# Kernel tuning notes

Measured on AMD Instinct MI355X. Metric: run time of the kernel, lower is better.

Reference implementation:

```python
import jax, jax.numpy as jnp
import numpy as np

N_NODES = 20000
N_EDGES = 120000
N_GRAPHS = 512
F_IN = 300
NHID = 256
NHID_FF = 256
NOUT = 768
SLOPE = 0.2
EPS = 1e-16


def _p(key, shape, scale=0.05):
    return jax.random.normal(key, shape, dtype=jnp.float32) * scale


def setup_inputs() -> dict:
    key = jax.random.key(0)
    ks = jax.random.split(key, 24)
    inp = {
        "x": jax.random.normal(ks[0], (N_NODES, F_IN), dtype=jnp.float32),
        "edge_index": jax.random.randint(ks[1], (2, N_EDGES), 0, N_NODES, dtype=jnp.int64) if False else jax.random.randint(ks[1], (2, N_EDGES), 0, N_NODES).astype(jnp.int32),
        "batch": jnp.sort(jax.random.randint(ks[2], (N_NODES,), 0, N_GRAPHS)).astype(jnp.int32),
        # conv1: in=300 -> heads=4, C=256, concat
        "c1_wl": _p(ks[3], (4 * NHID, F_IN)),
        "c1_wr": _p(ks[4], (4 * NHID, F_IN)),
        "c1_att": _p(ks[5], (4, NHID)),
        "c1_b": jnp.zeros((4 * NHID,), jnp.float32),
        # conv2: in=1024 -> heads=4, C=256, concat
        "c2_wl": _p(ks[6], (4 * NHID, 4 * NHID)),
        "c2_wr": _p(ks[7], (4 * NHID, 4 * NHID)),
        "c2_att": _p(ks[8], (4, NHID)),
        "c2_b": jnp.zeros((4 * NHID,), jnp.float32),
        # conv3: in=1024 -> heads=6, C=256, mean (concat=False)
        "c3_wl": _p(ks[9], (6 * NHID_FF, 4 * NHID)),
        "c3_wr": _p(ks[10], (6 * NHID_FF, 4 * NHID)),
        "c3_att": _p(ks[11], (6, NHID_FF)),
        "c3_b": jnp.zeros((NHID_FF,), jnp.float32),
        # post-process MLP
        "fp1_w": _p(ks[12], (NHID_FF, NHID_FF)),
        "fp1_b": jnp.zeros((NHID_FF,), jnp.float32),
        "fp2_w": _p(ks[13], (NOUT, NHID_FF)),
        "fp2_b": jnp.zeros((NOUT,), jnp.float32),
    }
    return inp


def gatv2(x, src, dst, wl, wr, att, b, concat):
    """GATv2Conv (PyG semantics, eval mode): lin_l on source, lin_r on target,
    score = att . leaky_relu(xl_j + xr_i), segment softmax over dst, aggregate xl_j."""
    n = x.shape[0]
    H, C = att.shape
    xl = (x @ wl.T).reshape(n, H, C)
    xr = (x @ wr.T).reshape(n, H, C)
    s = xl[src] + xr[dst]                                   # [E,H,C] gather
    s = jnp.where(s > 0, s, SLOPE * s)                      # leaky_relu
    scores = jnp.einsum("ehc,hc->eh", s, att)               # [E,H]
    mx = jax.ops.segment_max(scores, dst, num_segments=n)   # [N,H]
    ex = jnp.exp(scores - mx[dst])
    denom = jax.ops.segment_sum(ex, dst, num_segments=n)
    alpha = ex / (denom[dst] + EPS)                         # [E,H]
    out = jax.ops.segment_sum(alpha[:, :, None] * xl[src], dst, num_segments=n)  # [N,H,C]
    out = out.reshape(n, H * C) if concat else out.mean(axis=1)
    return out + b


def reference(x, edge_index, batch, c1_wl, c1_wr, c1_att, c1_b,
              c2_wl, c2_wr, c2_att, c2_b, c3_wl, c3_wr, c3_att, c3_b,
              fp1_w, fp1_b, fp2_w, fp2_b):
    n = x.shape[0]
    # PyG GATv2Conv defaults add_self_loops=True
    loops = jnp.arange(n, dtype=edge_index.dtype)
    src = jnp.concatenate([edge_index[0], loops])
    dst = jnp.concatenate([edge_index[1], loops])

    h = jax.nn.elu(gatv2(x, src, dst, c1_wl, c1_wr, c1_att, c1_b, concat=True))
    h = jax.nn.elu(gatv2(h, src, dst, c2_wl, c2_wr, c2_att, c2_b, concat=True))
    h = gatv2(h, src, dst, c3_wl, c3_wr, c3_att, c3_b, concat=False)

    # F.normalize(p=2, dim=-1), torch eps=1e-12
    norm = jnp.linalg.norm(h, axis=-1, keepdims=True)
    h = h / jnp.maximum(norm, 1e-12)

    # global_mean_pool over `batch`
    sums = jax.ops.segment_sum(h, batch, num_segments=N_GRAPHS)
    cnts = jax.ops.segment_sum(jnp.ones((n,), h.dtype), batch, num_segments=N_GRAPHS)
    pooled = sums / jnp.maximum(cnts, 1.0)[:, None]

    h = jax.nn.relu(pooled @ fp1_w.T + fp1_b)
    return h @ fp2_w.T + fp2_b
```

## Files before the change

kernel.cpp:

```cpp
#include <hip/hip_runtime.h>

typedef _Float16 h16;
typedef _Float16 h16x2 __attribute__((ext_vector_type(2)));
typedef _Float16 h16x4 __attribute__((ext_vector_type(4)));
typedef _Float16 h16x8 __attribute__((ext_vector_type(8)));
typedef float f32x4 __attribute__((ext_vector_type(4)));

static constexpr int NN   = 20000;
static constexpr int NPAD = 20224;
static constexpr int NE0  = 120000;
static constexpr int NE   = 140000;
static constexpr int NG   = 512;
static constexpr int FIN  = 300;
static constexpr int K1P  = 384;
static constexpr int CD   = 256;
static constexpr float SLOPE = 0.2f;

#define GLDS16(gsrc, ldst)                                                              \
  __builtin_amdgcn_global_load_lds(                                                    \
      (const __attribute__((address_space(1))) unsigned int*)(gsrc),                    \
      (__attribute__((address_space(3))) unsigned int*)(ldst), 16, 0, 0)

__global__ __launch_bounds__(256) void fill_x_kernel(const float* __restrict__ x, h16* __restrict__ a1) {
  int r = blockIdx.x;
  for (int c = threadIdx.x; c < K1P; c += 256) {
    float v = (r < NN && c < FIN) ? x[(size_t)r * FIN + c] : 0.f;
    a1[(size_t)r * K1P + c] = (h16)v;
  }
}

__global__ __launch_bounds__(256) void conv_w2_kernel(const float* __restrict__ wl, const float* __restrict__ wr,
                                                      h16* __restrict__ o, int rows, int cols, int colsp) {
  int r = blockIdx.x;
  const float* s = (r < rows) ? (wl + (size_t)r * cols) : (wr + (size_t)(r - rows) * cols);
  for (int c = threadIdx.x; c < colsp; c += 256) {
    float v = (c < cols) ? s[c] : 0.f;
    o[(size_t)r * colsp + c] = (h16)v;
  }
}

__global__ __launch_bounds__(256) void attcvt_kernel(const float* __restrict__ a, h16* __restrict__ o, int n) {
  int i = blockIdx.x * 256 + threadIdx.x;
  if (i < n) o[i] = (h16)a[i];
}

__global__ __launch_bounds__(256) void build_edges_kernel(const int* __restrict__ ei,
                                                          int* __restrict__ src, int* __restrict__ dst) {
  int e = blockIdx.x * 256 + threadIdx.x;
  if (e >= NE) return;
  if (e < NE0) { src[e] = ei[e]; dst[e] = ei[NE0 + e]; }
  else         { src[e] = e - NE0; dst[e] = e - NE0; }
}

__global__ __launch_bounds__(256) void deg_kernel(const int* __restrict__ dst, int* __restrict__ deg) {
  int e = blockIdx.x * 256 + threadIdx.x;
  if (e < NE) atomicAdd(&deg[dst[e]], 1);
}

__global__ __launch_bounds__(1024) void scan_kernel(const int* __restrict__ deg, int* __restrict__ rowptr) {
  __shared__ int b0[1024], b1[1024];
  __shared__ int carry;
  int t = threadIdx.x;
  if (t == 0) carry = 0;
  __syncthreads();
  for (int base = 0; base < NN; base += 1024) {
    int x = (base + t < NN) ? deg[base + t] : 0;
    b0[t] = x;
    __syncthreads();
    int* cur = b0; int* nxt = b1;
    for (int off = 1; off < 1024; off <<= 1) {
      int v = cur[t];
      if (t >= off) v += cur[t - off];
      nxt[t] = v;
      __syncthreads();
      int* tmp = cur; cur = nxt; nxt = tmp;
    }
    if (base + t < NN) rowptr[base + t] = carry + cur[t] - x;
    __syncthreads();
    if (t == 0) carry += cur[1023];
    __syncthreads();
  }
  if (t == 0) rowptr[NN] = carry;
}

__global__ __launch_bounds__(256) void scatter_kernel(const int* __restrict__ src, const int* __restrict__ dst,
                                                      const int* __restrict__ rowptr, int* __restrict__ cursor,
                                                      int* __restrict__ esrc) {
  int e = blockIdx.x * 256 + threadIdx.x;
  if (e >= NE) return;
  int d = dst[e];
  int pos = rowptr[d] + atomicAdd(&cursor[d], 1);
  esrc[pos] = src[e];
}

__global__ __launch_bounds__(512, 2) void gemm256_kernel(const h16* __restrict__ A, const h16* __restrict__ B,
                                                         h16* __restrict__ Co, int K, int Nw, int ntN) {
  __shared__ __align__(16) h16 lds[4 * 16384];
  int nwg = gridDim.x;
  int q = nwg >> 3, r = nwg & 7;
  int xc = blockIdx.x & 7, idx = blockIdx.x >> 3;
  int logical = (xc < r ? xc * (q + 1) : r * (q + 1) + (xc - r) * q) + idx;
  int tm = (logical / ntN) * 256, tn = (logical % ntN) * 256;

  int tid = threadIdx.x;
  int wv = tid >> 6, lane = tid & 63;
  int wm = (wv >> 2) * 128, wn = (wv & 3) * 64;
  int lrow = lane & 15, kq = lane >> 4, lr7 = lrow & 7;

  int rowoff = tid >> 3;
  int ug = ((tid & 7) ^ (rowoff & 7)) * 8;
  int ldsoff = (tid >> 6) * 512;

  const int NT = K >> 6;

  auto STAGE = [&](int buf, int kt) {
#pragma unroll
    for (int j = 0; j < 4; ++j) {
      GLDS16(A + (size_t)(tm + j * 64 + rowoff) * K + kt * 64 + ug,
             &lds[(buf * 2 + 0) * 16384 + j * 4096 + ldsoff]);
      GLDS16(B + (size_t)(tn + j * 64 + rowoff) * K + kt * 64 + ug,
             &lds[(buf * 2 + 1) * 16384 + j * 4096 + ldsoff]);
    }
  };

  STAGE(0, 0);
  STAGE(1, 1);

  f32x4 acc[8][4] = {};
  for (int t = 0; t < NT; ++t) {
    int b = t & 1;
    if (t + 1 < NT) { asm volatile("s_waitcnt vmcnt(8)" ::: "memory"); }
    else            { asm volatile("s_waitcnt vmcnt(0)" ::: "memory"); }
    __builtin_amdgcn_s_barrier();

    const h16* As_ = &lds[(b * 2 + 0) * 16384];
    const h16* Bs_ = &lds[(b * 2 + 1) * 16384];
    h16x8 af[8], bf[4];
#pragma unroll
    for (int i = 0; i < 8; ++i) af[i] = *(const h16x8*)&As_[(wm + i * 16 + lrow) * 64 + ((kq ^ lr7) * 8)];
#pragma unroll
    for (int j = 0; j < 4; ++j) bf[j] = *(const h16x8*)&Bs_[(wn + j * 16 + lrow) * 64 + ((kq ^ lr7) * 8)];
#pragma unroll
    for (int i = 0; i < 8; ++i)
#pragma unroll
      for (int j = 0; j < 4; ++j)
        acc[i][j] = __builtin_amdgcn_mfma_f32_16x16x32_f16(af[i], bf[j], acc[i][j], 0, 0, 0);
#pragma unroll
    for (int i = 0; i < 8; ++i) af[i] = *(const h16x8*)&As_[(wm + i * 16 + lrow) * 64 + (((4 + kq) ^ lr7) * 8)];
#pragma unroll
    for (int j = 0; j < 4; ++j) bf[j] = *(const h16x8*)&Bs_[(wn + j * 16 + lrow) * 64 + (((4 + kq) ^ lr7) * 8)];
    asm volatile("s_waitcnt lgkmcnt(0)" ::: "memory");
    __builtin_amdgcn_sched_barrier(0);
    __builtin_amdgcn_s_barrier();
    if (t + 2 < NT) STAGE(b, t + 2);
    __builtin_amdgcn_s_setprio(1);
#pragma unroll
    for (int i = 0; i < 8; ++i)
#pragma unroll
      for (int j = 0; j < 4; ++j)
        acc[i][j] = __builtin_amdgcn_mfma_f32_16x16x32_f16(af[i], bf[j], acc[i][j], 0, 0, 0);
    __builtin_amdgcn_s_setprio(0);
  }

  int cr = kq * 4, cc = lrow;
#pragma unroll
  for (int i = 0; i < 8; ++i)
#pragma unroll
    for (int j = 0; j < 4; ++j) {
      size_t base = (size_t)(tm + wm + i * 16 + cr) * Nw + (tn + wn + j * 16 + cc);
#pragma unroll
      for (int qq = 0; qq < 4; qq++) Co[base + (size_t)qq * Nw] = (h16)acc[i][j][qq];
    }
}

template <int H, int MODE>
__global__ __launch_bounds__(256) void sagg_kernel(
    const h16* __restrict__ X, const int* __restrict__ rowptr, const int* __restrict__ esrc,
    const h16* __restrict__ attH, const float* __restrict__ bias,
    h16* __restrict__ outA, const int* __restrict__ batch,
    float* __restrict__ pooled, int* __restrict__ cnt) {
  constexpr int NS = H / 2;
  constexpr int HC = H * CD;
  constexpr unsigned ROWB = (unsigned)(4 * HC);
  int n = blockIdx.x * 4 + (threadIdx.x >> 6);
  if (n >= NN) return;
  int lane = threadIdx.x & 63;
  unsigned lby = (unsigned)lane * 16u;
  const char* Xb = (const char*)X;
  unsigned nrow = (unsigned)n * ROWB;
  int beg = rowptr[n], end = rowptr[n + 1];

  float t8[8];
  if (MODE == 1) {
#pragma unroll
    for (int j = 0; j < 8; ++j) t8[j] = 0.f;
  }

  for (int s = 0; s < NS; ++s) {
    unsigned sby = (unsigned)s * 1024u + lby;
    h16x8 xr8 = *(const h16x8*)(Xb + nrow + (unsigned)(2 * HC) + sby);
    h16x8 aw8 = *(const h16x8*)((const char*)attH + sby);
    float m = -1e30f, den = 0.f;
    float acc[8] = {0.f, 0.f, 0.f, 0.f, 0.f, 0.f, 0.f, 0.f};

    for (int i = beg; i < end; i += 8) {
      int cn = end - i; if (cn > 8) cn = 8;
      unsigned offs[8];
#pragma unroll
      for (int k = 0; k < 8; ++k) {
        int idx = i + k; if (idx > end - 1) idx = end - 1;
        offs[k] = (unsigned)esrc[idx] * ROWB + sby;
      }
      h16x8 xv[8];
#pragma unroll
      for (int k = 0; k < 8; ++k) xv[k] = *(const h16x8*)(Xb + offs[k]);
      float ps[8];
#pragma unroll
      for (int k = 0; k < 8; ++k) {
        h16x8 v = xv[k] + xr8;
        h16x8 u = v * (h16)SLOPE;
        v = __builtin_elementwise_max(v, u);
        float p = 0.f;
        p = __builtin_amdgcn_fdot2(__builtin_shufflevector(v, v, 0, 1),
                                   __builtin_shufflevector(aw8, aw8, 0, 1), p, false);
        p = __builtin_amdgcn_fdot2(__builtin_shufflevector(v, v, 2, 3),
                                   __builtin_shufflevector(aw8, aw8, 2, 3), p, false);
        p = __builtin_amdgcn_fdot2(__builtin_shufflevector(v, v, 4, 5),
                                   __builtin_shufflevector(aw8, aw8, 4, 5), p, false);
        p = __builtin_amdgcn_fdot2(__builtin_shufflevector(v, v, 6, 7),
                                   __builtin_shufflevector(aw8, aw8, 6, 7), p, false);
        p += __shfl_xor(p, 1);  p += __shfl_xor(p, 2);  p += __shfl_xor(p, 4);
        p += __shfl_xor(p, 8);  p += __shfl_xor(p, 16);
        ps[k] = p;
      }
      float pm = ps[0];
#pragma unroll
      for (int k = 1; k < 8; ++k) pm = fmaxf(pm, ps[k]);
      float nm = fmaxf(m, pm);
      float f = __expf(m - nm);
      den *= f;
#pragma unroll
      for (int j = 0; j < 8; ++j) acc[j] *= f;
#pragma unroll
      for (int k = 0; k < 8; ++k) {
        float we = (k < cn) ? __expf(ps[k] - nm) : 0.f;
        den += we;
#pragma unroll
        for (int j = 0; j < 8; ++j) acc[j] += we * (float)xv[k][j];
      }
      m = nm;
    }
    float inv = 1.f / (den + 1e-16f);

    if (MODE == 0) {
      const float* bp = bias + s * 512 + lane * 8;
      float4 b0 = *(const float4*)bp;
      float4 b1 = *(const float4*)(bp + 4);
      const float* bb = (const float*)&b0;
      const float* bb2 = (const float*)&b1;
      h16x8 ov;
#pragma unroll
      for (int j = 0; j < 8; ++j) {
        float o = acc[j] * inv + (j < 4 ? bb[j] : bb2[j - 4]);
        o = o > 0.f ? o : expm1f(o);
        ov[j] = (h16)o;
      }
      *(h16x8*)(outA + (unsigned)n * HC + s * 512 + lane * 8) = ov;
    } else {
#pragma unroll
      for (int j = 0; j < 8; ++j) t8[j] += acc[j] * inv;
    }
  }

  if (MODE == 1) {
#pragma unroll
    for (int j = 0; j < 8; ++j) t8[j] += __shfl_xor(t8[j], 32);
    int cc = (lane & 31) * 8;
    float4 b0 = *(const float4*)(bias + cc);
    float4 b1 = *(const float4*)(bias + cc + 4);
    const float* bb = (const float*)&b0;
    const float* bb2 = (const float*)&b1;
    float ss = 0.f;
#pragma unroll
    for (int j = 0; j < 8; ++j) {
      t8[j] = t8[j] * (1.f / H) + (j < 4 ? bb[j] : bb2[j - 4]);
      ss += t8[j] * t8[j];
    }
    ss += __shfl_xor(ss, 1);  ss += __shfl_xor(ss, 2);  ss += __shfl_xor(ss, 4);
    ss += __shfl_xor(ss, 8);  ss += __shfl_xor(ss, 16);
    float scale = 1.f / fmaxf(sqrtf(ss), 1e-12f);
    int g = batch[n];
    if (lane < 32) {
#pragma unroll
      for (int j = 0; j < 8; ++j) atomicAdd(&pooled[(unsigned)g * CD + cc + j], t8[j] * scale);
    }
    if (lane == 0) atomicAdd(&cnt[g], 1);
  }
}

__global__ __launch_bounds__(256) void pool_div_kernel(float* __restrict__ pooled, const int* __restrict__ cnt) {
  int g = blockIdx.x, t = threadIdx.x;
  pooled[(size_t)g * CD + t] /= fmaxf((float)cnt[g], 1.f);
}

__global__ __launch_bounds__(256) void mlp1_kernel(const float* __restrict__ pooled, const float* __restrict__ w,
                                                   const float* __restrict__ b, float* __restrict__ hid) {
  __shared__ float xs[CD];
  int g = blockIdx.x, t = threadIdx.x;
  xs[t] = pooled[(size_t)g * CD + t];
  __syncthreads();
  float acc = b[t];
  for (int k = 0; k < CD; ++k) acc += xs[k] * w[(size_t)t * CD + k];
  hid[(size_t)g * CD + t] = fmaxf(acc, 0.f);
}

__global__ __launch_bounds__(256) void mlp2_kernel(const float* __restrict__ hid, const float* __restrict__ w,
                                                   const float* __restrict__ b, float* __restrict__ out) {
  __shared__ float xs[CD];
  int g = blockIdx.x, t = threadIdx.x;
  xs[t] = hid[(size_t)g * CD + t];
  __syncthreads();
  for (int o = t; o < 768; o += 256) {
    float acc = b[o];
    for (int k = 0; k < CD; ++k) acc += xs[k] * w[(size_t)o * CD + k];
    out[(size_t)g * 768 + o] = acc;
  }
}

extern "C" void kernel_launch(void* const* d_in, const int* in_sizes, int n_in,
                              void* d_out, int out_size, void* d_ws, size_t ws_size,
                              hipStream_t stream) {
  const float* x      = (const float*)d_in[0];
  const int*   ei     = (const int*)d_in[1];
  const int*   batch  = (const int*)d_in[2];
  const float* c1_wl  = (const float*)d_in[3];
  const float* c1_wr  = (const float*)d_in[4];
  const float* c1_att = (const float*)d_in[5];
  const float* c1_b   = (const float*)d_in[6];
  const float* c2_wl  = (const float*)d_in[7];
  const float* c2_wr  = (const float*)d_in[8];
  const float* c2_att = (const float*)d_in[9];
  const float* c2_b   = (const float*)d_in[10];
  const float* c3_wl  = (const float*)d_in[11];
  const float* c3_wr  = (const float*)d_in[12];
  const float* c3_att = (const float*)d_in[13];
  const float* c3_b   = (const float*)d_in[14];
  const float* fp1_w  = (const float*)d_in[15];
  const float* fp1_b  = (const float*)d_in[16];
  const float* fp2_w  = (const float*)d_in[17];
  const float* fp2_b  = (const float*)d_in[18];

  char* p = (char*)d_ws;
  size_t off = 0;
  auto alloc = [&](size_t b) { void* r = p + off; off += (b + 255) & ~(size_t)255; return r; };
  h16*  A    = (h16*)alloc((size_t)NPAD * 1024 * 2);
  h16*  Xa   = (h16*)alloc((size_t)NPAD * 3072 * 2);
  h16*  Xb   = (h16*)alloc((size_t)NPAD * 2048 * 2);
  h16*  A1   = Xb;
  h16*  W1   = (h16*)alloc((size_t)2048 * K1P * 2);
  h16*  W2   = (h16*)alloc((size_t)2048 * 1024 * 2);
  h16*  W3   = (h16*)alloc((size_t)3072 * 1024 * 2);
  h16*  attH1 = (h16*)alloc((size_t)4 * CD * 2);
  h16*  attH2 = (h16*)alloc((size_t)4 * CD * 2);
  h16*  attH3 = (h16*)alloc((size_t)6 * CD * 2);
  int*  srcA   = (int*)alloc((size_t)NE * 4);
  int*  dstA   = (int*)alloc((size_t)NE * 4);
  int*  esrc   = (int*)alloc((size_t)NE * 4);
  int*  deg    = (int*)alloc((size_t)NN * 4);
  int*  cursor = (int*)alloc((size_t)NN * 4);
  int*  rowptr = (int*)alloc((size_t)(NN + 1) * 4);
  float* pooled = (float*)alloc((size_t)NG * CD * 4);
  int*  cnt    = (int*)alloc((size_t)NG * 4);
  float* hid   = (float*)alloc((size_t)NG * CD * 4);

  hipMemsetAsync(deg, 0, (size_t)NN * 4, stream);
  hipMemsetAsync(cursor, 0, (size_t)NN * 4, stream);
  hipMemsetAsync(pooled, 0, (size_t)NG * CD * 4, stream);
  hipMemsetAsync(cnt, 0, (size_t)NG * 4, stream);

  fill_x_kernel<<<NPAD, 256, 0, stream>>>(x, A1);
  conv_w2_kernel<<<2048, 256, 0, stream>>>(c1_wl, c1_wr, W1, 1024, FIN, K1P);
  conv_w2_kernel<<<2048, 256, 0, stream>>>(c2_wl, c2_wr, W2, 1024, 1024, 1024);
  conv_w2_kernel<<<3072, 256, 0, stream>>>(c3_wl, c3_wr, W3, 1536, 1024, 1024);
  attcvt_kernel<<<4, 256, 0, stream>>>(c1_att, attH1, 4 * CD);
  attcvt_kernel<<<4, 256, 0, stream>>>(c2_att, attH2, 4 * CD);
  attcvt_kernel<<<6, 256, 0, stream>>>(c3_att, attH3, 6 * CD);

  int eb = (NE + 255) / 256;
  build_edges_kernel<<<eb, 256, 0, stream>>>(ei, srcA, dstA);
  deg_kernel<<<eb, 256, 0, stream>>>(dstA, deg);
  scan_kernel<<<1, 1024, 0, stream>>>(deg, rowptr);
  scatter_kernel<<<eb, 256, 0, stream>>>(srcA, dstA, rowptr, cursor, esrc);

  int sb = (NN + 3) / 4;

  gemm256_kernel<<<79 * 8, 512, 0, stream>>>(A1, W1, Xa, K1P, 2048, 8);
  sagg_kernel<4, 0><<<sb, 256, 0, stream>>>(Xa, rowptr, esrc, attH1, c1_b, A, nullptr, nullptr, nullptr);

  gemm256_kernel<<<79 * 8, 512, 0, stream>>>(A, W2, Xb, 1024, 2048, 8);
  sagg_kernel<4, 0><<<sb, 256, 0, stream>>>(Xb, rowptr, esrc, attH2, c2_b, A, nullptr, nullptr, nullptr);

  gemm256_kernel<<<79 * 12, 512, 0, stream>>>(A, W3, Xa, 1024, 3072, 12);
  sagg_kernel<6, 1><<<sb, 256, 0, stream>>>(Xa, rowptr, esrc, attH3, c3_b, nullptr, batch, pooled, cnt);

  pool_div_kernel<<<NG, 256, 0, stream>>>(pooled, cnt);
  mlp1_kernel<<<NG, 256, 0, stream>>>(pooled, fp1_w, fp1_b, hid);
  mlp2_kernel<<<NG, 256, 0, stream>>>(hid, fp2_w, fp2_b, (float*)d_out);
}
```

Baseline: 810.0 us.

## Split head-pair segments across warps in GATv2 aggregation kernel

Each node's head-pair slices now go to separate warps. A block handles 2 nodes with H/2 warps each, where before one warp looped serially over all slices of its node. This gives 2-3x more parallel warps for the latency-bound gather loops, at the cost of re-reading rowptr/esrc per warp. In mean mode, cross-warp head averaging and the L2 norm now run through shared memory with __syncthreads before the pooled atomics.

```diff
diff --git a/kernel.cpp b/kernel.cpp
--- a/kernel.cpp
+++ b/kernel.cpp
@@ -174,7 +174,7 @@
 }
 
 template <int H, int MODE>
-__global__ __launch_bounds__(256) void sagg_kernel(
+__global__ __launch_bounds__(64 * H) void sagg_kernel(
     const h16* __restrict__ X, const int* __restrict__ rowptr, const int* __restrict__ esrc,
     const h16* __restrict__ attH, const float* __restrict__ bias,
     h16* __restrict__ outA, const int* __restrict__ batch,
@@ -182,119 +182,119 @@
   constexpr int NS = H / 2;
   constexpr int HC = H * CD;
   constexpr unsigned ROWB = (unsigned)(4 * HC);
-  int n = blockIdx.x * 4 + (threadIdx.x >> 6);
-  if (n >= NN) return;
-  int lane = threadIdx.x & 63;
-  unsigned lby = (unsigned)lane * 16u;
+  int tid = threadIdx.x;
+  int w = tid >> 6, lane = tid & 63;
+  int k = w / NS, s = w - k * NS;
+  int n = blockIdx.x * 2 + k;
+  unsigned sby = (unsigned)s * 1024u + (unsigned)lane * 16u;
   const char* Xb = (const char*)X;
   unsigned nrow = (unsigned)n * ROWB;
+
+  h16x8 xr8 = *(const h16x8*)(Xb + nrow + (unsigned)(2 * HC) + sby);
+  h16x8 aw8 = *(const h16x8*)((const char*)attH + sby);
   int beg = rowptr[n], end = rowptr[n + 1];
 
-  float t8[8];
-  if (MODE == 1) {
-#pragma unroll
-    for (int j = 0; j < 8; ++j) t8[j] = 0.f;
-  }
-
-  for (int s = 0; s < NS; ++s) {
-    unsigned sby = (unsigned)s * 1024u + lby;
-    h16x8 xr8 = *(const h16x8*)(Xb + nrow + (unsigned)(2 * HC) + sby);
-    h16x8 aw8 = *(const h16x8*)((const char*)attH + sby);
-    float m = -1e30f, den = 0.f;
-    float acc[8] = {0.f, 0.f, 0.f, 0.f, 0.f, 0.f, 0.f, 0.f};
-
-    for (int i = beg; i < end; i += 8) {
-      int cn = end - i; if (cn > 8) cn = 8;
-      unsigned offs[8];
-#pragma unroll
-      for (int k = 0; k < 8; ++k) {
-        int idx = i + k; if (idx > end - 1) idx = end - 1;
-        offs[k] = (unsigned)esrc[idx] * ROWB + sby;
-      }
-      h16x8 xv[8];
-#pragma unroll
-      for (int k = 0; k < 8; ++k) xv[k] = *(const h16x8*)(Xb + offs[k]);
-      float ps[8];
-#pragma unroll
-      for (int k = 0; k < 8; ++k) {
-        h16x8 v = xv[k] + xr8;
-        h16x8 u = v * (h16)SLOPE;
-        v = __builtin_elementwise_max(v, u);
-        float p = 0.f;
-        p = __builtin_amdgcn_fdot2(__builtin_shufflevector(v, v, 0, 1),
-                                   __builtin_shufflevector(aw8, aw8, 0, 1), p, false);
-        p = __builtin_amdgcn_fdot2(__builtin_shufflevector(v, v, 2, 3),
-                                   __builtin_shufflevector(aw8, aw8, 2, 3), p, false);
-        p = __builtin_amdgcn_fdot2(__builtin_shufflevector(v, v, 4, 5),
-                                   __builtin_shufflevector(aw8, aw8, 4, 5), p, false);
-        p = __builtin_amdgcn_fdot2(__builtin_shufflevector(v, v, 6, 7),
-                                   __builtin_shufflevector(aw8, aw8, 6, 7), p, false);
-        p += __shfl_xor(p, 1);  p += __shfl_xor(p, 2);  p += __shfl_xor(p, 4);
-        p += __shfl_xor(p, 8);  p += __shfl_xor(p, 16);
-        ps[k] = p;
-      }
-      float pm = ps[0];
-#pragma unroll
-      for (int k = 1; k < 8; ++k) pm = fmaxf(pm, ps[k]);
-      float nm = fmaxf(m, pm);
-      float f = __expf(m - nm);
-      den *= f;
-#pragma unroll
-      for (int j = 0; j < 8; ++j) acc[j] *= f;
-#pragma unroll
-      for (int k = 0; k < 8; ++k) {
-        float we = (k < cn) ? __expf(ps[k] - nm) : 0.f;
-        den += we;
-#pragma unroll
-        for (int j = 0; j < 8; ++j) acc[j] += we * (float)xv[k][j];
-      }
-      m = nm;
-    }
-    float inv = 1.f / (den + 1e-16f);
-
-    if (MODE == 0) {
-      const float* bp = bias + s * 512 + lane * 8;
-      float4 b0 = *(const float4*)bp;
-      float4 b1 = *(const float4*)(bp + 4);
-      const float* bb = (const float*)&b0;
-      const float* bb2 = (const float*)&b1;
-      h16x8 ov;
-#pragma unroll
-      for (int j = 0; j < 8; ++j) {
-        float o = acc[j] * inv + (j < 4 ? bb[j] : bb2[j - 4]);
-        o = o > 0.f ? o : expm1f(o);
-        ov[j] = (h16)o;
-      }
-      *(h16x8*)(outA + (unsigned)n * HC + s * 512 + lane * 8) = ov;
-    } else {
-#pragma unroll
-      for (int j = 0; j < 8; ++j) t8[j] += acc[j] * inv;
-    }
-  }
-
-  if (MODE == 1) {
-#pragma unroll
-    for (int j = 0; j < 8; ++j) t8[j] += __shfl_xor(t8[j], 32);
-    int cc = (lane & 31) * 8;
-    float4 b0 = *(const float4*)(bias + cc);
-    float4 b1 = *(const float4*)(bias + cc + 4);
+  float m = -1e30f, den = 0.f;
+  float acc[8] = {0.f, 0.f, 0.f, 0.f, 0.f, 0.f, 0.f, 0.f};
+
+  for (int i = beg; i < end; i += 8) {
+    int cn = end - i; if (cn > 8) cn = 8;
+    unsigned offs[8];
+#pragma unroll
+    for (int kk = 0; kk < 8; ++kk) {
+      int idx = i + kk; if (idx > end - 1) idx = end - 1;
+      offs[kk] = (unsigned)esrc[idx] * ROWB + sby;
+    }
+    h16x8 xv[8];
+#pragma unroll
+    for (int kk = 0; kk < 8; ++kk) xv[kk] = *(const h16x8*)(Xb + offs[kk]);
+    float ps[8];
+#pragma unroll
+    for (int kk = 0; kk < 8; ++kk) {
+      h16x8 v = xv[kk] + xr8;
+      h16x8 u = v * (h16)SLOPE;
+      v = __builtin_elementwise_max(v, u);
+      float p = 0.f;
+      p = __builtin_amdgcn_fdot2(__builtin_shufflevector(v, v, 0, 1),
+                                 __builtin_shufflevector(aw8, aw8, 0, 1), p, false);
+      p = __builtin_amdgcn_fdot2(__builtin_shufflevector(v, v, 2, 3),
+                                 __builtin_shufflevector(aw8, aw8, 2, 3), p, false);
+      p = __builtin_amdgcn_fdot2(__builtin_shufflevector(v, v, 4, 5),
+                                 __builtin_shufflevector(aw8, aw8, 4, 5), p, false);
+      p = __builtin_amdgcn_fdot2(__builtin_shufflevector(v, v, 6, 7),
+                                 __builtin_shufflevector(aw8, aw8, 6, 7), p, false);
+      p += __shfl_xor(p, 1);  p += __shfl_xor(p, 2);  p += __shfl_xor(p, 4);
+      p += __shfl_xor(p, 8);  p += __shfl_xor(p, 16);
+      ps[kk] = p;
+    }
+    float pm = ps[0];
+#pragma unroll
+    for (int kk = 1; kk < 8; ++kk) pm = fmaxf(pm, ps[kk]);
+    float nm = fmaxf(m, pm);
+    float f = __expf(m - nm);
+    den *= f;
+#pragma unroll
+    for (int j = 0; j < 8; ++j) acc[j] *= f;
+#pragma unroll
+    for (int kk = 0; kk < 8; ++kk) {
+      float we = (kk < cn) ? __expf(ps[kk] - nm) : 0.f;
+      den += we;
+#pragma unroll
+      for (int j = 0; j < 8; ++j) acc[j] += we * (float)xv[kk][j];
+    }
+    m = nm;
+  }
+  float inv = 1.f / (den + 1e-16f);
+
+  if (MODE == 0) {
+    const float* bp = bias + s * 512 + lane * 8;
+    float4 b0 = *(const float4*)bp;
+    float4 b1 = *(const float4*)(bp + 4);
     const float* bb = (const float*)&b0;
     const float* bb2 = (const float*)&b1;
-    float ss = 0.f;
+    h16x8 ov;
 #pragma unroll
     for (int j = 0; j < 8; ++j) {
-      t8[j] = t8[j] * (1.f / H) + (j < 4 ? bb[j] : bb2[j - 4]);
-      ss += t8[j] * t8[j];
-    }
-    ss += __shfl_xor(ss, 1);  ss += __shfl_xor(ss, 2);  ss += __shfl_xor(ss, 4);
-    ss += __shfl_xor(ss, 8);  ss += __shfl_xor(ss, 16);
-    float scale = 1.f / fmaxf(sqrtf(ss), 1e-12f);
-    int g = batch[n];
+      float o = acc[j] * inv + (j < 4 ? bb[j] : bb2[j - 4]);
+      o = o > 0.f ? o : expm1f(o);
+      ov[j] = (h16)o;
+    }
+    *(h16x8*)(outA + (unsigned)n * HC + s * 512 + lane * 8) = ov;
+  } else {
+    __shared__ float sacc[2][NS][32][8];
+    __shared__ float spart[2][2 * NS];
+    float t8[8];
+#pragma unroll
+    for (int j = 0; j < 8; ++j) {
+      t8[j] = acc[j] * inv;
+      t8[j] += __shfl_xor(t8[j], 32);
+    }
     if (lane < 32) {
 #pragma unroll
-      for (int j = 0; j < 8; ++j) atomicAdd(&pooled[(unsigned)g * CD + cc + j], t8[j] * scale);
-    }
-    if (lane == 0) atomicAdd(&cnt[g], 1);
+      for (int j = 0; j < 8; ++j) sacc[k][s][lane][j] = t8[j];
+    }
+    __syncthreads();
+#pragma unroll
+    for (int kk = 0; kk < 2; ++kk) {
+      float mv = 0.f;
+      if (tid < CD) {
+#pragma unroll
+        for (int s2 = 0; s2 < NS; ++s2) mv += sacc[kk][s2][tid >> 3][tid & 7];
+        mv = mv * (1.f / H) + bias[tid];
+      }
+      float ss = (tid < CD) ? mv * mv : 0.f;
+      ss += __shfl_xor(ss, 1);  ss += __shfl_xor(ss, 2);  ss += __shfl_xor(ss, 4);
+      ss += __shfl_xor(ss, 8);  ss += __shfl_xor(ss, 16); ss += __shfl_xor(ss, 32);
+      if (lane == 0) spart[kk][w] = ss;
+      __syncthreads();
+      float tot = 0.f;
+#pragma unroll
+      for (int ww = 0; ww < 2 * NS; ++ww) tot += spart[kk][ww];
+      float scale = 1.f / fmaxf(sqrtf(tot), 1e-12f);
+      int g = batch[blockIdx.x * 2 + kk];
+      if (tid < CD) atomicAdd(&pooled[(unsigned)g * CD + tid], mv * scale);
+      if (tid == 0) atomicAdd(&cnt[g], 1);
+    }
   }
 }
 
@@ -392,7 +392,7 @@
   scan_kernel<<<1, 1024, 0, stream>>>(deg, rowptr);
   scatter_kernel<<<eb, 256, 0, stream>>>(srcA, dstA, rowptr, cursor, esrc);
 
-  int sb = (NN + 3) / 4;
+  int sb = NN / 2;
 
   gemm256_kernel<<<79 * 8, 512, 0, stream>>>(A1, W1, Xa, K1P, 2048, 8);
   sagg_kernel<4, 0><<<sb, 256, 0, stream>>>(Xa, rowptr, esrc, attH1, c1_b, A, nullptr, nullptr, nullptr);
@@ -401,7 +401,7 @@
   sagg_kernel<4, 0><<<sb, 256, 0, stream>>>(Xb, rowptr, esrc, attH2, c2_b, A, nullptr, nullptr, nullptr);
 
   gemm256_kernel<<<79 * 12, 512, 0, stream>>>(A, W3, Xa, 1024, 3072, 12);
-  sagg_kernel<6, 1><<<sb, 256, 0, stream>>>(Xa, rowptr, esrc, attH3, c3_b, nullptr, batch, pooled, cnt);
+  sagg_kernel<6, 1><<<sb, 384, 0, stream>>>(Xa, rowptr, esrc, attH3, c3_b, nullptr, batch, pooled, cnt);
 
   pool_div_kernel<<<NG, 256, 0, stream>>>(pooled, cnt);
   mlp1_kernel<<<NG, 256, 0, stream>>>(pooled, fp1_w, fp1_b, hid);
```

Measured after the change: 782.2 us. 1.04x faster.
